# Optimization experiments

Hardware: AMD Instinct MI355X
Metric: run time of the kernel (lower is better)

## Reference

```python
import jax, jax.numpy as jnp
import numpy as np

L, H, P = 16384, 256, 512


def setup_inputs() -> dict:
    key = jax.random.key(0)
    ks = jax.random.split(key, 7)
    return {
        "input_sequence": jax.random.normal(ks[0], (L, H), jnp.float32),
        "A_diag": jax.random.normal(ks[1], (P,), jnp.float32) * 2.0,
        "G_diag": jax.random.uniform(ks[2], (P,), jnp.float32),  # in [0,1): keeps 1 - sigmoid(dt)*G > 0
        "dt": jax.random.normal(ks[3], (P,), jnp.float32) * 0.5,
        "B": jax.random.uniform(ks[4], (P, H, 2), jnp.float32, -1.0, 1.0) / np.sqrt(H).astype(np.float32),
        "C": jax.random.uniform(ks[5], (H, P, 2), jnp.float32, -1.0, 1.0) / np.sqrt(P).astype(np.float32),
        "D": jax.random.normal(ks[6], (H,), jnp.float32),
    }


def _combine(q_i, q_j):
    # q = (A, b); A: (..., 4, P) real 2x2 block-diagonal entries [A,B,C,D], b: (..., 2, P) complex
    A_i, b_i = q_i
    A_j, b_j = q_j
    iA, iB, iC, iD = A_i[..., 0, :], A_i[..., 1, :], A_i[..., 2, :], A_i[..., 3, :]
    jA, jB, jC, jD = A_j[..., 0, :], A_j[..., 1, :], A_j[..., 2, :], A_j[..., 3, :]
    A_new = jnp.stack(
        [jA * iA + jB * iC, jA * iB + jB * iD, jC * iA + jD * iC, jC * iB + jD * iD],
        axis=-2,
    )
    b1, b2 = b_i[..., 0, :], b_i[..., 1, :]
    b_new = jnp.stack([jA * b1 + jB * b2, jC * b1 + jD * b2], axis=-2) + b_j
    return (A_new, b_new)


def reference(input_sequence, A_diag, G_diag, dt, B, C, D):
    # complex parameter assembly
    B_c = B[..., 0] + 1j * B[..., 1]      # (P, H) complex
    C_c = C[..., 0] + 1j * C[..., 1]      # (H, P) complex

    # _soft_project_AGdt
    dts = jax.nn.sigmoid(dt)
    G = jax.nn.relu(G_diag)
    root = jnp.sqrt(1.0 - dts * G)
    denom = jnp.maximum(dts ** 2, 1e-6)
    A_low = (2.0 - dts * G - 2.0 * root) / denom
    A_high = (2.0 - dts * G + 2.0 * root) / denom
    A = A_low + jax.nn.relu(A_diag - A_low) - jax.nn.relu(A_diag - A_high)

    # Bu_k = B_complex @ u_k for all k: (L, P) complex64
    Bu = input_sequence.astype(B_c.dtype) @ B_c.T

    # IMEX2 transition matrix (diagonal 2x2 blocks), constant over time
    M = jnp.stack(
        [1.0 - dts * G, -dts * A, dts * (1.0 - dts * G), 1.0 - dts ** 2 * A],
        axis=0,
    )  # (4, P)
    seq_len = input_sequence.shape[0]
    M_el = jnp.broadcast_to(M, (seq_len, 4, M.shape[-1]))          # (L, 4, P)
    F = jnp.stack([dts * Bu, dts ** 2 * Bu], axis=1)               # (L, 2, P) complex

    _, xs = jax.lax.associative_scan(_combine, (M_el, F))
    ys = xs[:, 1, :]                                                # x-component, (L, P) complex

    out = (ys @ C_c.T).real.astype(input_sequence.dtype) + input_sequence * D
    return out
```

## Files before the change

### kernel.cpp

```cpp
#include <hip/hip_runtime.h>
#include <math.h>

#define L_SEQ 16384
#define H_DIM 256
#define P_DIM 512
#define CL 32
#define NC (L_SEQ / CL)

typedef __attribute__((ext_vector_type(8))) short bf16x8;
typedef __attribute__((ext_vector_type(4))) float f32x4;

static __device__ __forceinline__ unsigned short f2bf(float f) {
  unsigned int u = __builtin_bit_cast(unsigned int, f);
  u += 0x7FFFu + ((u >> 16) & 1u);
  return (unsigned short)(u >> 16);
}
static __device__ __forceinline__ float bflo(unsigned int v) {
  return __builtin_bit_cast(float, v << 16);
}
static __device__ __forceinline__ float bfhi(unsigned int v) {
  return __builtin_bit_cast(float, v & 0xFFFF0000u);
}
static __device__ __forceinline__ float bf2f(unsigned short s) {
  return __builtin_bit_cast(float, (unsigned int)s << 16);
}

__global__ __launch_bounds__(256) void prep_all(
    const float* __restrict__ A_diag, const float* __restrict__ G_diag,
    const float* __restrict__ dt, const float* __restrict__ B,
    const float* __restrict__ C, const float* __restrict__ u,
    float* __restrict__ prm, unsigned short* __restrict__ W1b,
    unsigned short* __restrict__ W2b, unsigned short* __restrict__ ub) {
  const int b = blockIdx.x;
  const int t = threadIdx.x;
  if (b < 2) {
    int p = b * 256 + t;
    float dts = 1.0f / (1.0f + expf(-dt[p]));
    float G = fmaxf(G_diag[p], 0.0f);
    float g = dts * G;
    float root = sqrtf(1.0f - g);
    float denom = fmaxf(dts * dts, 1e-6f);
    float A_low  = (2.0f - g - 2.0f * root) / denom;
    float A_high = (2.0f - g + 2.0f * root) / denom;
    float Ad = A_diag[p];
    float A = A_low + fmaxf(Ad - A_low, 0.0f) - fmaxf(Ad - A_high, 0.0f);
    float m00 = 1.0f - g;
    float m01 = -dts * A;
    float m10 = dts * (1.0f - g);
    float m11 = 1.0f - dts * dts * A;
    float c00 = m00, c01 = m01, c10 = m10, c11 = m11;
#pragma unroll
    for (int i = 0; i < 5; i++) {
      float n00 = c00 * c00 + c01 * c10;
      float n01 = c00 * c01 + c01 * c11;
      float n10 = c10 * c00 + c11 * c10;
      float n11 = c10 * c01 + c11 * c11;
      c00 = n00; c01 = n01; c10 = n10; c11 = n11;
    }
    prm[0 * P_DIM + p] = m00;
    prm[1 * P_DIM + p] = m01;
    prm[2 * P_DIM + p] = m10;
    prm[3 * P_DIM + p] = m11;
    prm[4 * P_DIM + p] = dts;
    prm[5 * P_DIM + p] = dts * dts;
    prm[6 * P_DIM + p] = c00;
    prm[7 * P_DIM + p] = c01;
    prm[8 * P_DIM + p] = c10;
    prm[9 * P_DIM + p] = c11;
  } else if (b < 2 + 1024) {
    int idx = (b - 2) * 256 + t;
    int n = idx >> 8;
    int k = idx & 255;
    int p = n >> 1, c = n & 1;
    W1b[((size_t)(k >> 3) * 1024 + n) * 8 + (k & 7)] = f2bf(B[(p * H_DIM + k) * 2 + c]);
  } else if (b < 2 + 2048) {
    int idx = (b - 1026) * 256 + t;
    int h = idx >> 10;
    int k = idx & 1023;
    int p = k >> 1, c = k & 1;
    float v = C[(h * P_DIM + p) * 2 + c];
    W2b[((size_t)(k >> 3) * 256 + h) * 8 + (k & 7)] = f2bf(c ? -v : v);
  } else {
    int idx = (b - 2050) * 256 + t;
    float4 v = ((const float4*)u)[idx];
    ushort4 o;
    o.x = f2bf(v.x); o.y = f2bf(v.y); o.z = f2bf(v.z); o.w = f2bf(v.w);
    ((ushort4*)ub)[idx] = o;
  }
}

__global__ __launch_bounds__(256) void gemm1_scan(
    const unsigned short* __restrict__ A, const unsigned short* __restrict__ W,
    unsigned short* __restrict__ Out,
    const float* __restrict__ prm, float4* __restrict__ finals) {
  constexpr int N = 1024, K = H_DIM;
  __shared__ unsigned short tA[128 * 32];
  __shared__ unsigned short tW[128 * 32];
  __shared__ unsigned short stg[128 * 132];
  const int tid = threadIdx.x;
  const int lane = tid & 63;
  const int wid = tid >> 6;
  const int wr = wid >> 1;
  const int wc = wid & 1;
  const int bm = blockIdx.x * 128;
  const int bn = blockIdx.y * 128;

  f32x4 acc[4][4] = {};
  const int rA = lane & 15;
  const int g = lane >> 4;

  for (int k0 = 0; k0 < K; k0 += 32) {
    __syncthreads();
#pragma unroll
    for (int c = wid; c < 8; c += 4) {
      const int unit = c * 64 + lane;
      const int kg = unit >> 7, r = unit & 127;
      const unsigned short* src = A + ((size_t)(bm + r) * 32 + (k0 >> 3) + kg) * 8;
      __builtin_amdgcn_global_load_lds(
          (const __attribute__((address_space(1))) void*)src,
          (__attribute__((address_space(3))) void*)(tA + c * 512), 16, 0, 0);
    }
#pragma unroll
    for (int c = wid; c < 8; c += 4) {
      const int unit = c * 64 + lane;
      const int kg = unit >> 7, n = unit & 127;
      const unsigned short* src = W + ((size_t)((k0 >> 3) + kg) * 1024 + bn + n) * 8;
      __builtin_amdgcn_global_load_lds(
          (const __attribute__((address_space(1))) void*)src,
          (__attribute__((address_space(3))) void*)(tW + c * 512), 16, 0, 0);
    }
    __syncthreads();

    bf16x8 af[4], wf[4];
#pragma unroll
    for (int i = 0; i < 4; i++)
      af[i] = *(const bf16x8*)&tA[(g * 128 + wr * 64 + i * 16 + rA) * 8];
#pragma unroll
    for (int j = 0; j < 4; j++)
      wf[j] = *(const bf16x8*)&tW[(g * 128 + wc * 64 + j * 16 + rA) * 8];
#pragma unroll
    for (int i = 0; i < 4; i++)
#pragma unroll
      for (int j = 0; j < 4; j++)
        acc[i][j] = __builtin_amdgcn_mfma_f32_16x16x32_bf16(af[i], wf[j], acc[i][j], 0, 0, 0);
  }

  const int cr = (lane >> 4) * 4;
  const int cc = lane & 15;
#pragma unroll
  for (int i = 0; i < 4; i++)
#pragma unroll
    for (int j = 0; j < 4; j++) {
      const int rl = wr * 64 + i * 16 + cr;
      const int clc = wc * 64 + j * 16 + cc;
#pragma unroll
      for (int q = 0; q < 4; q++) {
        const unsigned short hv = f2bf(acc[i][j][q]);
        Out[(size_t)(bm + rl + q) * N + bn + clc] = hv;
        stg[(rl + q) * 132 + clc] = hv;
      }
    }

  __syncthreads();
  {
    const int i = tid >> 6;
    const int pl = tid & 63;
    const int p = (bn >> 1) + pl;
    const int cglob = blockIdx.x * 4 + i;
    float m00 = prm[0 * P_DIM + p], m01 = prm[1 * P_DIM + p];
    float m10 = prm[2 * P_DIM + p], m11 = prm[3 * P_DIM + p];
    float dts = prm[4 * P_DIM + p], dts2 = prm[5 * P_DIM + p];
    float x1r = 0.f, x2r = 0.f, x1i = 0.f, x2i = 0.f;
    const unsigned int* stg32 = (const unsigned int*)stg;
#pragma unroll 8
    for (int s = 0; s < CL; s++) {
      unsigned int v = stg32[(i * 32 + s) * 66 + pl];
      float bx = bflo(v), by = bfhi(v);
      float n1r = fmaf(m00, x1r, fmaf(m01, x2r, dts * bx));
      float n2r = fmaf(m10, x1r, fmaf(m11, x2r, dts2 * bx));
      float n1i = fmaf(m00, x1i, fmaf(m01, x2i, dts * by));
      float n2i = fmaf(m10, x1i, fmaf(m11, x2i, dts2 * by));
      x1r = n1r; x2r = n2r; x1i = n1i; x2i = n2i;
    }
    finals[(size_t)cglob * P_DIM + p] = make_float4(x1r, x2r, x1i, x2i);
  }
}

__global__ __launch_bounds__(NC) void scan_carry(
    const float4* __restrict__ finals, const float* __restrict__ prm,
    float4* __restrict__ carry) {
  int p = blockIdx.x;
  int c = threadIdx.x;
  __shared__ float4 sb[NC];
  float m00 = prm[6 * P_DIM + p], m01 = prm[7 * P_DIM + p];
  float m10 = prm[8 * P_DIM + p], m11 = prm[9 * P_DIM + p];
  float4 b = finals[c * P_DIM + p];
  for (int o = 1; o < NC; o <<= 1) {
    sb[c] = b;
    __syncthreads();
    float4 nb = (c >= o) ? sb[c - o] : make_float4(0.f, 0.f, 0.f, 0.f);
    __syncthreads();
    b.x = fmaf(m00, nb.x, fmaf(m01, nb.y, b.x));
    b.y = fmaf(m10, nb.x, fmaf(m11, nb.y, b.y));
    b.z = fmaf(m00, nb.z, fmaf(m01, nb.w, b.z));
    b.w = fmaf(m10, nb.z, fmaf(m11, nb.w, b.w));
    float n00 = m00 * m00 + m01 * m10;
    float n01 = m00 * m01 + m01 * m11;
    float n10 = m10 * m00 + m11 * m10;
    float n11 = m10 * m01 + m11 * m11;
    m00 = n00; m01 = n01; m10 = n10; m11 = n11;
  }
  if (c + 1 < NC) carry[(c + 1) * P_DIM + p] = b;
  if (c == 0) carry[p] = make_float4(0.f, 0.f, 0.f, 0.f);
}

__global__ __launch_bounds__(256) void gemm2_fused(
    const unsigned int* __restrict__ Bu16, const float* __restrict__ prm,
    const float4* __restrict__ carry, const unsigned short* __restrict__ W2b,
    const unsigned short* __restrict__ ub, const float* __restrict__ Dv,
    float* __restrict__ out) {
  extern __shared__ char smem[];
  unsigned int* yA = (unsigned int*)smem;
  unsigned short* tW0 = (unsigned short*)smem;
  unsigned short* tW1 = (unsigned short*)(smem + 16384);
  const int tid = threadIdx.x;
  const int lane = tid & 63;
  const int wid = tid >> 6;
  const int row0 = blockIdx.x * 32;

#pragma unroll
  for (int h = 0; h < 2; h++) {
    const int p = tid + h * 256;
    float m00 = prm[0 * P_DIM + p], m01 = prm[1 * P_DIM + p];
    float m10 = prm[2 * P_DIM + p], m11 = prm[3 * P_DIM + p];
    float dts = prm[4 * P_DIM + p], dts2 = prm[5 * P_DIM + p];
    float4 s = carry[(size_t)blockIdx.x * P_DIM + p];
    float x1r = s.x, x2r = s.y, x1i = s.z, x2i = s.w;
    const unsigned int* src = Bu16 + (size_t)row0 * P_DIM + p;
#pragma unroll 8
    for (int i = 0; i < 32; i++) {
      unsigned int v = src[(size_t)i * P_DIM];
      float bx = bflo(v), by = bfhi(v);
      float n1r = fmaf(m00, x1r, fmaf(m01, x2r, dts * bx));
      float n2r = fmaf(m10, x1r, fmaf(m11, x2r, dts2 * bx));
      float n1i = fmaf(m00, x1i, fmaf(m01, x2i, dts * by));
      float n2i = fmaf(m10, x1i, fmaf(m11, x2i, dts2 * by));
      yA[(i * 512 + p) ^ ((i & 7) << 2)] =
          (unsigned int)f2bf(n2r) | ((unsigned int)f2bf(n2i) << 16);
      x1r = n1r; x2r = n2r; x1i = n1i; x2i = n2i;
    }
  }
  __syncthreads();

  const int wr = wid >> 1;
  const int wc = wid & 1;
  const int rA = lane & 15;
  const int g = lane >> 4;
  const int kc = g * 8;
  const int arow = wr * 16 + rA;
  const unsigned short* yAs = (const unsigned short*)yA;
  bf16x8 af[32];
#pragma unroll
  for (int t = 0; t < 32; t++)
    af[t] = *(const bf16x8*)&yAs[((unsigned)(arow * 1024 + t * 32 + kc)) ^ ((arow & 7) << 3)];
  __syncthreads();

  auto STAGE = [&](unsigned short* buf, int k0) {
#pragma unroll
    for (int c = wid; c < 16; c += 4) {
      const unsigned short* src = W2b + ((size_t)(k0 >> 3) * 256 + c * 64 + lane) * 8;
      __builtin_amdgcn_global_load_lds(
          (const __attribute__((address_space(1))) void*)src,
          (__attribute__((address_space(3))) void*)(buf + c * 512), 16, 0, 0);
    }
  };

  f32x4 acc[8] = {};
  STAGE(tW0, 0);
  __syncthreads();
#pragma unroll
  for (int t = 0; t < 32; t++) {
    const unsigned short* cur = (t & 1) ? tW1 : tW0;
    unsigned short* nxt = (t & 1) ? tW0 : tW1;
    if (t < 31) STAGE(nxt, (t + 1) * 32);
#pragma unroll
    for (int j = 0; j < 8; j++) {
      bf16x8 wf = *(const bf16x8*)&cur[(g * 256 + wc * 128 + j * 16 + rA) * 8];
      acc[j] = __builtin_amdgcn_mfma_f32_16x16x32_bf16(af[t], wf, acc[j], 0, 0, 0);
    }
    __syncthreads();
  }

  const int cr = (lane >> 4) * 4;
  const int cc = lane & 15;
#pragma unroll
  for (int j = 0; j < 8; j++) {
    const int col = wc * 128 + j * 16 + cc;
    const float d = Dv[col];
#pragma unroll
    for (int q = 0; q < 4; q++) {
      const int row = row0 + wr * 16 + cr + q;
      const size_t idx = (size_t)row * H_DIM + col;
      out[idx] = fmaf(bf2f(ub[idx]), d, acc[j][q]);
    }
  }
}

extern "C" void kernel_launch(void* const* d_in, const int* in_sizes, int n_in,
                              void* d_out, int out_size, void* d_ws, size_t ws_size,
                              hipStream_t stream) {
  const float* u      = (const float*)d_in[0];
  const float* A_diag = (const float*)d_in[1];
  const float* G_diag = (const float*)d_in[2];
  const float* dt     = (const float*)d_in[3];
  const float* B      = (const float*)d_in[4];
  const float* C      = (const float*)d_in[5];
  const float* D      = (const float*)d_in[6];
  float* out = (float*)d_out;

  char* w = (char*)d_ws;
  unsigned short* Bu16 = (unsigned short*)w;
  unsigned short* ub   = (unsigned short*)(w + (size_t)L_SEQ * 1024 * 2);
  unsigned short* W1b  = ub + (size_t)L_SEQ * H_DIM;
  unsigned short* W2b  = W1b + 1024 * H_DIM;
  float* prm    = (float*)(W2b + H_DIM * 1024);
  float* finals = prm + 8192;
  float* carryb = finals + (size_t)NC * P_DIM * 4;

  prep_all<<<2 + 1024 + 1024 + 4096, 256, 0, stream>>>(
      A_diag, G_diag, dt, B, C, u, prm, W1b, W2b, ub);

  gemm1_scan<<<dim3(L_SEQ / 128, 1024 / 128), 256, 0, stream>>>(
      ub, W1b, Bu16, prm, (float4*)finals);

  scan_carry<<<P_DIM, NC, 0, stream>>>(
      (const float4*)finals, prm, (float4*)carryb);

  gemm2_fused<<<L_SEQ / 32, 256, 65536, stream>>>(
      (const unsigned int*)Bu16, prm, (const float4*)carryb, W2b, ub, D, out);
}
```

Before: 72.67 us.

## Load W2 fragments directly from global instead of double-buffered LDS staging

```diff
diff --git a/kernel.cpp b/kernel.cpp
--- a/kernel.cpp
+++ b/kernel.cpp
@@ -219,10 +219,7 @@
     const float4* __restrict__ carry, const unsigned short* __restrict__ W2b,
     const unsigned short* __restrict__ ub, const float* __restrict__ Dv,
     float* __restrict__ out) {
-  extern __shared__ char smem[];
-  unsigned int* yA = (unsigned int*)smem;
-  unsigned short* tW0 = (unsigned short*)smem;
-  unsigned short* tW1 = (unsigned short*)(smem + 16384);
+  __shared__ unsigned int yA[32 * 512];
   const int tid = threadIdx.x;
   const int lane = tid & 63;
   const int wid = tid >> 6;
@@ -256,39 +253,19 @@
   const int wc = wid & 1;
   const int rA = lane & 15;
   const int g = lane >> 4;
-  const int kc = g * 8;
   const int arow = wr * 16 + rA;
   const unsigned short* yAs = (const unsigned short*)yA;
-  bf16x8 af[32];
-#pragma unroll
-  for (int t = 0; t < 32; t++)
-    af[t] = *(const bf16x8*)&yAs[((unsigned)(arow * 1024 + t * 32 + kc)) ^ ((arow & 7) << 3)];
-  __syncthreads();
-
-  auto STAGE = [&](unsigned short* buf, int k0) {
-#pragma unroll
-    for (int c = wid; c < 16; c += 4) {
-      const unsigned short* src = W2b + ((size_t)(k0 >> 3) * 256 + c * 64 + lane) * 8;
-      __builtin_amdgcn_global_load_lds(
-          (const __attribute__((address_space(1))) void*)src,
-          (__attribute__((address_space(3))) void*)(buf + c * 512), 16, 0, 0);
-    }
-  };
-
+  const unsigned short* wbase = W2b + ((size_t)g * 256 + wc * 128 + rA) * 8;
   f32x4 acc[8] = {};
-  STAGE(tW0, 0);
-  __syncthreads();
-#pragma unroll
+
+#pragma unroll 4
   for (int t = 0; t < 32; t++) {
-    const unsigned short* cur = (t & 1) ? tW1 : tW0;
-    unsigned short* nxt = (t & 1) ? tW0 : tW1;
-    if (t < 31) STAGE(nxt, (t + 1) * 32);
+    bf16x8 af = *(const bf16x8*)&yAs[((unsigned)(arow * 1024 + t * 32 + g * 8)) ^ ((arow & 7) << 3)];
 #pragma unroll
     for (int j = 0; j < 8; j++) {
-      bf16x8 wf = *(const bf16x8*)&cur[(g * 256 + wc * 128 + j * 16 + rA) * 8];
-      acc[j] = __builtin_amdgcn_mfma_f32_16x16x32_bf16(af[t], wf, acc[j], 0, 0, 0);
-    }
-    __syncthreads();
+      bf16x8 wf = *(const bf16x8*)&wbase[(size_t)t * 8192 + j * 128];
+      acc[j] = __builtin_amdgcn_mfma_f32_16x16x32_bf16(af, wf, acc[j], 0, 0, 0);
+    }
   }
 
   const int cr = (lane >> 4) * 4;
@@ -336,6 +313,6 @@
   scan_carry<<<P_DIM, NC, 0, stream>>>(
       (const float4*)finals, prm, (float4*)carryb);
 
-  gemm2_fused<<<L_SEQ / 32, 256, 65536, stream>>>(
+  gemm2_fused<<<L_SEQ / 32, 256, 0, stream>>>(
       (const unsigned int*)Bu16, prm, (const float4*)carryb, W2b, ub, D, out);
 }
```

Result: slower. 79.99 us (+10.1%).
